# Optimization experiments

Measured on AMD Instinct MI355X. Metric: run time of the kernel, lower is better.

Reference implementation:

```python
import jax, jax.numpy as jnp
import numpy as np

PATCH, WIN = 3, 7


def _unfold(x, k):
    # torch F.unfold(x, k, padding=k//2), stride 1 -> [b, c, k*k, h, w]
    # channel-major ordering (c slowest, then kernel row, then kernel col)
    pad = k // 2
    b, c, h, w = x.shape
    xp = jnp.pad(x, ((0, 0), (0, 0), (pad, pad), (pad, pad)))
    return jnp.stack([xp[:, :, i:i + h, j:j + w]
                      for i in range(k) for j in range(k)], axis=2)


def _conv3(x, w, b=None):
    y = jax.lax.conv_general_dilated(x, w, (1, 1), [(1, 1), (1, 1)],
                                     dimension_numbers=('NCHW', 'OIHW', 'NCHW'))
    if b is not None:
        y = y + b[None, :, None, None]
    return y


def _head(u_feat, pan_feat, w_phi, w_theta, w_g, p, ws):
    # SelfAttention: windowed/patch neighborhood attention
    b, c, h, w = pan_feat.shape
    phi = jnp.einsum('oi,bihw->bohw', w_phi, pan_feat)
    theta = jnp.einsum('oi,bihw->bohw', w_theta, pan_feat)
    thp = _unfold(theta, p).reshape(b, c * p * p, h, w)        # [b,D,h,w]
    php = _unfold(phi, p).reshape(b, c * p * p, h, w)          # [b,D,h,w]
    phw = _unfold(php, ws)                                     # [b,D,K,h,w], K=ws*ws
    att = jax.nn.softmax(jnp.einsum('bdhw,bdkhw->bhwk', thp, phw), axis=-1)
    g = jnp.einsum('oi,bihw->bohw', w_g, u_feat)
    gw = _unfold(g, ws)                                        # [b,cu,K,h,w]
    return jnp.einsum('bhwk,bckhw->bchw', att, gw)


def _forward(u, pan, w_nlu, w_nlpan, g_phi, g_theta, g_g, s_phi, s_theta, s_g,
             m_phi, m_theta, m_g, mlp_w, mlp_b, w_resu, w_respan,
             rb0_w1, rb0_b1, rb0_w2, rb0_b2, rb1_w1, rb1_b1, rb1_w2, rb1_b2,
             rb2_w1, rb2_b1, rb2_w2, rb2_b2, w_recon):
    uf = _conv3(u, w_nlu)      # [b,5,h,w]
    pf = _conv3(pan, w_nlpan)  # [b,3,h,w]
    h1 = _head(uf, pf, g_phi, g_theta, g_g, PATCH, WIN)
    h2 = _head(uf, uf, s_phi, s_theta, s_g, 1, WIN)
    h3 = _head(uf, jnp.concatenate([uf, pf], axis=1), m_phi, m_theta, m_g, PATCH, WIN)
    # mlp: Linear(3,1) over stacked heads (last dim of size 3)
    att = h1 * mlp_w[0, 0] + h2 * mlp_w[0, 1] + h3 * mlp_w[0, 2] + mlp_b[0]
    ru = _conv3(u, w_resu)
    rp = _conv3(pan, w_respan)
    x = jnp.concatenate([att, ru, rp], axis=1)  # [b, fc+10, h, w]
    rbs = [(rb0_w1, rb0_b1, rb0_w2, rb0_b2),
           (rb1_w1, rb1_b1, rb1_w2, rb1_b2),
           (rb2_w1, rb2_b1, rb2_w2, rb2_b2)]
    for w1, b1, w2, b2 in rbs:
        f = jax.nn.relu(_conv3(x, w1, b1))
        f = _conv3(f, w2, b2)
        x = jax.nn.relu(f + x)
    return _conv3(x, w_recon)


def setup_inputs() -> dict:
    key = jax.random.key(0)
    ks = jax.random.split(key, 32)
    def n(i, shape, s=0.1):
        return jax.random.normal(ks[i], shape, dtype=jnp.float32) * s
    B, H, W = 1, 128, 128
    FC = 32
    C = FC + 10
    inp = {
        'u': jax.random.normal(ks[0], (B, 8, H, W), dtype=jnp.float32),
        'pan': jax.random.normal(ks[1], (B, 1, H, W), dtype=jnp.float32),
        'w_nlu': n(2, (5, 8, 3, 3)),
        'w_nlpan': n(3, (3, 1, 3, 3)),
        'g_phi': n(4, (3, 3)), 'g_theta': n(5, (3, 3)), 'g_g': n(6, (5, 5)),
        's_phi': n(7, (5, 5)), 's_theta': n(8, (5, 5)), 's_g': n(9, (5, 5)),
        'm_phi': n(10, (8, 8)), 'm_theta': n(11, (8, 8)), 'm_g': n(12, (5, 5)),
        'mlp_w': n(13, (1, 3), 0.5), 'mlp_b': n(14, (1,), 0.1),
        'w_resu': n(15, (FC, 8, 3, 3)), 'w_respan': n(16, (5, 1, 3, 3)),
        'w_recon': n(17, (8, C, 3, 3)),
    }
    k = 18
    for i in range(3):
        inp[f'rb{i}_w1'] = n(k, (C, C, 3, 3))
        inp[f'rb{i}_b1'] = n(k + 1, (C,), 0.01)
        inp[f'rb{i}_w2'] = n(k + 2, (C, C, 3, 3))
        inp[f'rb{i}_b2'] = n(k + 3, (C,), 0.01)
        k += 4
    return inp


def reference(u, pan, w_nlu, w_nlpan, g_phi, g_theta, g_g, s_phi, s_theta, s_g,
              m_phi, m_theta, m_g, mlp_w, mlp_b, w_resu, w_respan,
              rb0_w1, rb0_b1, rb0_w2, rb0_b2, rb1_w1, rb1_b1, rb1_w2, rb1_b2,
              rb2_w1, rb2_b1, rb2_w2, rb2_b2, w_recon):
    return _forward(u, pan, w_nlu, w_nlpan, g_phi, g_theta, g_g, s_phi, s_theta,
                    s_g, m_phi, m_theta, m_g, mlp_w, mlp_b, w_resu, w_respan,
                    rb0_w1, rb0_b1, rb0_w2, rb0_b2, rb1_w1, rb1_b1, rb1_w2,
                    rb1_b2, rb2_w1, rb2_b1, rb2_w2, rb2_b2, w_recon)
```

## Files before the change

### kernel.cpp

```cpp
#include <hip/hip_runtime.h>


#define DEV __device__ __forceinline__
typedef float f32x4 __attribute__((ext_vector_type(4)));
typedef __bf16 bf16x8 __attribute__((ext_vector_type(8)));
typedef unsigned short u16;
typedef unsigned int u32;

constexpr int N = 128 * 128;

constexpr int OFF_PHI1 =   0 * N;
constexpr int OFF_TH1  =   3 * N;
constexpr int OFF_PHI2 =   6 * N;
constexpr int OFF_TH2  =  11 * N;
constexpr int OFF_PHI3 =  16 * N;
constexpr int OFF_TH3  =  24 * N;
constexpr int OFF_G1   =  32 * N;
constexpr int OFF_G2   =  37 * N;
constexpr int OFF_G3   =  42 * N;
constexpr int OFF_X    =  47 * N;
constexpr int OFF_OH1  =  89 * N;
constexpr int OFF_OH2  =  94 * N;
constexpr int OFF_OH3  =  99 * N;
constexpr int XPLANE   = 130 * 136;
constexpr int OFF_XPAD = 110 * N;
constexpr int OFF_FPAD = 133 * N;
constexpr int OFF_SLAB = 156 * N;
constexpr int OFF_BTAB = 160 * N;
constexpr int SLAB_RB  = 18432;
constexpr int SLAB_RC  = 110592;
constexpr int SLAB_TOT = 116736;
constexpr int ZPB      = 528;
constexpr int ZTOT     = 2 * 42 * ZPB;
constexpr int WPREP_TOT = 384 + SLAB_TOT + ZTOT;
constexpr int WPREP_BLK = (WPREP_TOT + 255) / 256;

DEV bool inb(int y, int x) { return (unsigned)y < 128u && (unsigned)x < 128u; }
DEV u16 f2bf(float f) {
    unsigned u = __float_as_uint(f);
    return (u16)((u + 0x7fffu + ((u >> 16) & 1u)) >> 16);
}

struct PrepArgs {
    const float* u;    const float* pan;  const float* wnlu; const float* wnlpan;
    const float* gphi; const float* gth;  const float* gg;   const float* sphi;
    const float* sth;  const float* sg;   const float* mphi; const float* mth;
    const float* mg;
    const float* w[7];
};

__global__ __launch_bounds__(256) void prep_k(PrepArgs pa, float* __restrict__ ws,
                                              u16* __restrict__ slab,
                                              u16* __restrict__ btab,
                                              u16* __restrict__ xpad,
                                              u16* __restrict__ fpad) {
    const int bid = blockIdx.x, t = threadIdx.x;
    if (bid < 256) {
        const int g = bid >> 6;
        const int p = (bid & 63) * 256 + t;
        const int y = p >> 7, x = p & 127;

        float uv[8][9];
#pragma unroll
        for (int ic = 0; ic < 8; ++ic)
#pragma unroll
            for (int i = 0; i < 3; ++i)
#pragma unroll
                for (int j = 0; j < 3; ++j) {
                    int yy = y + i - 1, xx = x + j - 1;
                    uv[ic][i * 3 + j] =
                        inb(yy, xx) ? pa.u[ic * N + yy * 128 + xx] : 0.f;
                }
        float uf[5] = {0, 0, 0, 0, 0};
#pragma unroll
        for (int ic = 0; ic < 8; ++ic)
#pragma unroll
            for (int k = 0; k < 9; ++k)
#pragma unroll
                for (int o = 0; o < 5; ++o)
                    uf[o] = fmaf(uv[ic][k], pa.wnlu[(o * 8 + ic) * 9 + k], uf[o]);

        if (g == 0) {
#pragma unroll
            for (int o = 0; o < 5; ++o) {
                float a = 0, b = 0, c1 = 0;
#pragma unroll
                for (int i = 0; i < 5; ++i) {
                    a  = fmaf(pa.sphi[o * 5 + i], uf[i], a);
                    b  = fmaf(pa.sth [o * 5 + i], uf[i], b);
                    c1 = fmaf(pa.gg  [o * 5 + i], uf[i], c1);
                }
                ws[OFF_PHI2 + o * N + p] = a;
                ws[OFF_TH2  + o * N + p] = b;
                ws[OFF_G1   + o * N + p] = c1;
            }
        } else if (g == 1) {
#pragma unroll
            for (int o = 0; o < 5; ++o) {
                float c2 = 0, c3 = 0;
#pragma unroll
                for (int i = 0; i < 5; ++i) {
                    c2 = fmaf(pa.sg[o * 5 + i], uf[i], c2);
                    c3 = fmaf(pa.mg[o * 5 + i], uf[i], c3);
                }
                ws[OFF_G2 + o * N + p] = c2;
                ws[OFF_G3 + o * N + p] = c3;
            }
        } else {
            float pv[9];
#pragma unroll
            for (int i = 0; i < 3; ++i)
#pragma unroll
                for (int j = 0; j < 3; ++j) {
                    int yy = y + i - 1, xx = x + j - 1;
                    pv[i * 3 + j] = inb(yy, xx) ? pa.pan[yy * 128 + xx] : 0.f;
                }
            float pf[3] = {0, 0, 0};
#pragma unroll
            for (int k = 0; k < 9; ++k)
#pragma unroll
                for (int o = 0; o < 3; ++o)
                    pf[o] = fmaf(pv[k], pa.wnlpan[o * 9 + k], pf[o]);
            float cat[8] = {uf[0], uf[1], uf[2], uf[3], uf[4],
                            pf[0], pf[1], pf[2]};
            if (g == 2) {
#pragma unroll
                for (int o = 0; o < 3; ++o) {
                    float a = 0, b = 0;
#pragma unroll
                    for (int i = 0; i < 3; ++i) {
                        a = fmaf(pa.gphi[o * 3 + i], pf[i], a);
                        b = fmaf(pa.gth [o * 3 + i], pf[i], b);
                    }
                    ws[OFF_PHI1 + o * N + p] = a;
                    ws[OFF_TH1  + o * N + p] = b;
                }
#pragma unroll
                for (int o = 0; o < 8; ++o) {
                    float a = 0;
#pragma unroll
                    for (int i = 0; i < 8; ++i)
                        a = fmaf(pa.mphi[o * 8 + i], cat[i], a);
                    ws[OFF_PHI3 + o * N + p] = a;
                }
            } else {
#pragma unroll
                for (int o = 0; o < 8; ++o) {
                    float b = 0;
#pragma unroll
                    for (int i = 0; i < 8; ++i)
                        b = fmaf(pa.mth[o * 8 + i], cat[i], b);
                    ws[OFF_TH3 + o * N + p] = b;
                }
            }
        }
        return;
    }

    int idx = (bid - 256) * 256 + t;
    if (idx >= WPREP_TOT) return;
    if (idx < 384) {
        u16 v = 0;
        if (idx < 378) {
            int ic = idx / 9, tau = idx - ic * 9;
            v = (u16)(ic * 120 + (tau / 3) * 40 + (tau % 3));
        }
        btab[idx] = v;
        return;
    }
    idx -= 384;
    if (idx < SLAB_TOT) {
        const float* W;
        int mt, ks, lane, j, ocv;
        if (idx < SLAB_RC) {
            int cv = idx / SLAB_RB, r = idx - cv * SLAB_RB;
            mt = r / 6144; r -= mt * 6144;
            ks = r / 512;  r -= ks * 512;
            lane = r / 8;  j = r - lane * 8;
            W = pa.w[cv]; ocv = 42;
        } else {
            int r = idx - SLAB_RC;
            mt = 0;
            ks = r / 512;  r -= ks * 512;
            lane = r / 8;  j = r - lane * 8;
            W = pa.w[6]; ocv = 8;
        }
        int k  = ks * 32 + (lane >> 4) * 8 + j;
        int oc = mt * 16 + (lane & 15);
        u16 v = 0;
        if (k < 378 && oc < ocv) {
            int ic = k / 9, tau = k - ic * 9;
            v = f2bf(W[(oc * 42 + ic) * 9 + tau]);
        }
        slab[idx] = v;
        return;
    }
    idx -= SLAB_TOT;
    u16* buf = (idx < 42 * ZPB) ? xpad : fpad;
    int e = (idx < 42 * ZPB) ? idx : idx - 42 * ZPB;
    int plane = e / ZPB, rem = e - plane * ZPB;
    int row, col;
    if (rem < 136)      { row = 0;             col = rem; }
    else if (rem < 272) { row = 129;           col = rem - 136; }
    else if (rem < 400) { row = 1 + rem - 272; col = 0; }
    else                { row = 1 + rem - 400; col = 129; }
    buf[plane * XPLANE + row * 136 + col] = 0;
}

template <int C, int P>
DEV void head_tile(const float* __restrict__ phi, const float* __restrict__ theta,
                   const float* __restrict__ g, float* __restrict__ oh,
                   float* __restrict__ smem, int ty0, int tx0, int t) {
    constexpr int PR  = P / 2;
    constexpr int H3  = 3 + PR;
    constexpr int W   = 6 + P;
    constexpr int TTH = 8 + 2 * PR, TTW = 8 + 2 * PR;
    constexpr int PTH = 8 + 2 * H3, PTW = 8 + 2 * H3;
    constexpr int GTH = 14, GTW = 14;
    constexpr int CH0 = (C + 1) / 2;

    float* sT = smem;
    float* sP = sT + C * TTH * TTW;
    float* sG = sP + C * PTH * PTW;

#pragma unroll
    for (int c = 0; c < C; ++c) {
        int i = t;
        if (i < TTH * TTW) {
            int r = i / TTW, cc = i - r * TTW;
            int gy = ty0 - PR + r, gx = tx0 - PR + cc;
            sT[c * TTH * TTW + i] =
                inb(gy, gx) ? theta[c * N + gy * 128 + gx] : 0.f;
        }
    }
#pragma unroll
    for (int c = 0; c < C; ++c) {
        int i = t;
        if (i < PTH * PTW) {
            int r = i / PTW, cc = i - r * PTW;
            int gy = ty0 - H3 + r, gx = tx0 - H3 + cc;
            sP[c * PTH * PTW + i] =
                inb(gy, gx) ? phi[c * N + gy * 128 + gx] : 0.f;
        }
    }
#pragma unroll
    for (int c = 0; c < 5; ++c) {
        int i = t;
        if (i < GTH * GTW) {
            int r = i / GTW, cc = i - r * GTW;
            int gy = ty0 - 3 + r, gx = tx0 - 3 + cc;
            sG[c * GTH * GTW + i] =
                inb(gy, gx) ? g[c * N + gy * 128 + gx] : 0.f;
        }
    }
    __syncthreads();

    const int lane = t & 63, wave = t >> 6;
    const int h = (lane >> 4) & 1, m = lane >> 5;
    const int pidx = wave * 16 + (lane & 15);
    const int py = pidx >> 3, px = pidx & 7;
    const int gy = ty0 + py, gx = tx0 + px;
    const int dbase = m * 3;
    const int cbeg = h ? CH0 : 0, cend = h ? C : CH0;

    float s[28];
#pragma unroll
    for (int k = 0; k < 28; ++k) s[k] = 0.f;

#pragma unroll
    for (int ci = 0; ci < CH0; ++ci) {
        int c = cbeg + ci;
        bool cok = c < cend;
        const float* tc = sT + (cok ? c : 0) * TTH * TTW;
        const float* pc = sP + (cok ? c : 0) * PTH * PTW;
        float T[P][P];
#pragma unroll
        for (int i = 0; i < P; ++i)
#pragma unroll
            for (int j = 0; j < P; ++j)
                T[i][j] = cok ? tc[(py + i) * TTW + px + j] : 0.f;
        float R[P][W];
#pragma unroll
        for (int r = 0; r < P; ++r)
#pragma unroll
            for (int w = 0; w < W; ++w)
                R[r][w] = pc[(py + dbase + r) * PTW + px + w];
#pragma unroll
        for (int dd = 0; dd < 4; ++dd) {
#pragma unroll
            for (int dx = 0; dx < 7; ++dx) {
                float a = 0.f;
#pragma unroll
                for (int i = 0; i < P; ++i)
#pragma unroll
                    for (int j = 0; j < P; ++j)
                        a = fmaf(T[i][j], R[i][dx + j], a);
                s[dd * 7 + dx] += a;
            }
            if (dd < 3) {
#pragma unroll
                for (int r = 0; r < P - 1; ++r)
#pragma unroll
                    for (int w = 0; w < W; ++w) R[r][w] = R[r + 1][w];
                int row = py + dbase + dd + P;
#pragma unroll
                for (int w = 0; w < W; ++w)
                    R[P - 1][w] = pc[row * PTW + px + w];
            }
        }
    }
#pragma unroll
    for (int k = 0; k < 28; ++k) s[k] += __shfl_xor(s[k], 16);

#pragma unroll
    for (int k = 0; k < 28; ++k) {
        int d = dbase + k / 7, dx = k % 7;
        if (!inb(gy + d - 3, gx + dx - 3)) s[k] = 0.f;
    }
    const bool half0 = (m == 0);
    float mx = -3.0e38f;
#pragma unroll
    for (int k = 0; k < 28; ++k) {
        bool own = half0 || (k >= 7);
        mx = own ? fmaxf(mx, s[k]) : mx;
    }
    mx = fmaxf(mx, __shfl_xor(mx, 32));
    float sum = 0.f;
#pragma unroll
    for (int k = 0; k < 28; ++k) {
        bool own = half0 || (k >= 7);
        float e = own ? __expf(s[k] - mx) : 0.f;
        s[k] = e;
        sum += e;
    }
    sum += __shfl_xor(sum, 32);

    const int gb = h ? 3 : 0, gn = h ? 2 : 3;
    float o[3] = {0, 0, 0};
#pragma unroll
    for (int k = 0; k < 28; ++k) {
        int d = dbase + k / 7, dx = k % 7;
        int gr = (py + d) * GTW + px + dx;
#pragma unroll
        for (int c5 = 0; c5 < 3; ++c5)
            if (c5 < gn)
                o[c5] = fmaf(s[k], sG[(gb + c5) * GTH * GTW + gr], o[c5]);
    }
#pragma unroll
    for (int c5 = 0; c5 < 3; ++c5) o[c5] += __shfl_xor(o[c5], 32);

    if (half0) {
        float inv = 1.f / sum;
        int p = gy * 128 + gx;
#pragma unroll
        for (int c5 = 0; c5 < 3; ++c5)
            if (c5 < gn) oh[(gb + c5) * N + p] = o[c5] * inv;
    }
}

__global__ __launch_bounds__(256) void heads_k(float* __restrict__ ws) {
    __shared__ float smem[3828];
    const int t = threadIdx.x;
    const int ty0 = (blockIdx.x >> 4) * 8, tx0 = (blockIdx.x & 15) * 8;
    if (blockIdx.y == 0)
        head_tile<3, 3>(ws + OFF_PHI1, ws + OFF_TH1, ws + OFF_G1, ws + OFF_OH1,
                        smem, ty0, tx0, t);
    else if (blockIdx.y == 1)
        head_tile<5, 1>(ws + OFF_PHI2, ws + OFF_TH2, ws + OFF_G2, ws + OFF_OH2,
                        smem, ty0, tx0, t);
    else
        head_tile<8, 3>(ws + OFF_PHI3, ws + OFF_TH3, ws + OFF_G3, ws + OFF_OH3,
                        smem, ty0, tx0, t);
}

__global__ __launch_bounds__(256, 2) void assemble_k(
    const float* __restrict__ u, const float* __restrict__ pan,
    const float* __restrict__ wres, const float* __restrict__ wrp,
    const float* __restrict__ mlpw, const float* __restrict__ mlpb,
    float* __restrict__ ws, u16* __restrict__ xpad) {
    const int p = blockIdx.x * 256 + threadIdx.x;
    const int y = p >> 7, x = p & 127;
    const int padp = (y + 1) * 136 + (x + 1);
    float* xb = ws + OFF_X;

    if (blockIdx.y == 0) {
        const float w0 = mlpw[0], w1 = mlpw[1], w2 = mlpw[2];
        const float bb = mlpb[0];
#pragma unroll
        for (int c = 0; c < 5; ++c) {
            float a = ws[OFF_OH1 + c * N + p] * w0 +
                      ws[OFF_OH2 + c * N + p] * w1 +
                      ws[OFF_OH3 + c * N + p] * w2 + bb;
            xb[c * N + p] = a;
            xpad[c * XPLANE + padp] = f2bf(a);
        }
        float pv[9];
#pragma unroll
        for (int i = 0; i < 3; ++i)
#pragma unroll
            for (int j = 0; j < 3; ++j) {
                int yy = y + i - 1, xx = x + j - 1;
                pv[i * 3 + j] = inb(yy, xx) ? pan[yy * 128 + xx] : 0.f;
            }
        float a5[5] = {0, 0, 0, 0, 0};
#pragma unroll
        for (int k = 0; k < 9; ++k)
#pragma unroll
            for (int o = 0; o < 5; ++o)
                a5[o] = fmaf(pv[k], wrp[o * 9 + k], a5[o]);
#pragma unroll
        for (int o = 0; o < 5; ++o) {
            xb[(37 + o) * N + p] = a5[o];
            xpad[(37 + o) * XPLANE + padp] = f2bf(a5[o]);
        }
    } else {
        const int ob = (blockIdx.y - 1) * 8;
        float uv[8][9];
#pragma unroll
        for (int ic = 0; ic < 8; ++ic)
#pragma unroll
            for (int i = 0; i < 3; ++i)
#pragma unroll
                for (int j = 0; j < 3; ++j) {
                    int yy = y + i - 1, xx = x + j - 1;
                    uv[ic][i * 3 + j] =
                        inb(yy, xx) ? u[ic * N + yy * 128 + xx] : 0.f;
                }
        float acc[8] = {0, 0, 0, 0, 0, 0, 0, 0};
#pragma unroll
        for (int ic = 0; ic < 8; ++ic)
#pragma unroll
            for (int k = 0; k < 9; ++k)
#pragma unroll
                for (int o = 0; o < 8; ++o)
                    acc[o] = fmaf(uv[ic][k], wres[((ob + o) * 8 + ic) * 9 + k],
                                  acc[o]);
#pragma unroll
        for (int o = 0; o < 8; ++o) {
            xb[(5 + ob + o) * N + p] = acc[o];
            xpad[(5 + ob + o) * XPLANE + padp] = f2bf(acc[o]);
        }
    }
}

template <bool SKIP, bool WF32, bool WPAD>
__global__ __launch_bounds__(384, 3) void convm_k(
    const u16* __restrict__ xin, const u16* __restrict__ slab,
    const u16* __restrict__ btab, const float* __restrict__ bs,
    const float* __restrict__ skip, float* __restrict__ of32,
    u16* __restrict__ opad) {
    __shared__ __align__(16) u16 sX[5040];
    __shared__ __align__(16) u16 sBt[384];
    const int t = threadIdx.x;
    const int y = blockIdx.x >> 2, x0 = (blockIdx.x & 3) << 5;

    const u16* srcbase = xin + y * 136 + x0;
#pragma unroll
    for (int it = 0; it < 2; ++it) {
        int c = it * 384 + t;
        if (c < 630) {
            int row = c / 5, slot = c - row * 5;
            int ic = row / 3, r = row - ic * 3;
            uint4 v = *((const uint4*)(srcbase + ic * XPLANE + r * 136) + slot);
            *(uint4*)(sX + row * 40 + slot * 8) = v;
        }
    }
    sBt[t >= 384 ? 0 : t] = btab[t >= 384 ? 0 : t];
    __syncthreads();

    const int lane = t & 63, wave = t >> 6;
    const int ph = wave / 3, mt = wave - ph * 3;
    const int quad = lane >> 4, col = lane & 15;
    const int ncol = ph * 16 + col;

    union AB { uint4 u; bf16x8 b; };
    AB a[12];
#pragma unroll
    for (int ks = 0; ks < 12; ++ks)
        a[ks].u = ((const uint4*)slab)[(mt * 12 + ks) * 64 + lane];

    f32x4 acc = {0.f, 0.f, 0.f, 0.f};
#pragma unroll
    for (int ks = 0; ks < 12; ++ks) {
        union { uint4 u; u16 s[8]; } off;
        off.u = *(const uint4*)(sBt + ks * 32 + quad * 8);
        union { u16 s[8]; bf16x8 b; } bv;
#pragma unroll
        for (int j = 0; j < 8; ++j) bv.s[j] = sX[off.s[j] + ncol];
        acc = __builtin_amdgcn_mfma_f32_16x16x32_bf16(a[ks].b, bv.b, acc,
                                                      0, 0, 0);
    }

    const int xg = x0 + ncol;
    const int px = y * 128 + xg;
    const int padp = (y + 1) * 136 + (xg + 1);
#pragma unroll
    for (int reg = 0; reg < 4; ++reg) {
        int oc = mt * 16 + quad * 4 + reg;
        if (oc < 42) {
            float v = acc[reg] + bs[oc];
            if (SKIP) v += skip[oc * N + px];
            v = fmaxf(v, 0.f);
            if (WF32) of32[oc * N + px] = v;
            if (WPAD) opad[oc * XPLANE + padp] = f2bf(v);
        }
    }
}

__global__ __launch_bounds__(128, 1) void convr_k(
    const u16* __restrict__ xin, const u16* __restrict__ slab,
    const u16* __restrict__ btab, float* __restrict__ out) {
    __shared__ __align__(16) u16 sX[5040];
    __shared__ __align__(16) u16 sBt[384];
    const int t = threadIdx.x;
    const int y = blockIdx.x >> 2, x0 = (blockIdx.x & 3) << 5;

    const u16* srcbase = xin + y * 136 + x0;
#pragma unroll
    for (int it = 0; it < 5; ++it) {
        int c = it * 128 + t;
        if (c < 630) {
            int row = c / 5, slot = c - row * 5;
            int ic = row / 3, r = row - ic * 3;
            uint4 v = *((const uint4*)(srcbase + ic * XPLANE + r * 136) + slot);
            *(uint4*)(sX + row * 40 + slot * 8) = v;
        }
    }
#pragma unroll
    for (int it = 0; it < 3; ++it) sBt[it * 128 + t] = btab[it * 128 + t];
    __syncthreads();

    const int lane = t & 63, wave = t >> 6;
    const int quad = lane >> 4, col = lane & 15;
    const int ncol = wave * 16 + col;

    union AB { uint4 u; bf16x8 b; };
    AB a[12];
#pragma unroll
    for (int ks = 0; ks < 12; ++ks)
        a[ks].u = ((const uint4*)slab)[ks * 64 + lane];

    f32x4 acc = {0.f, 0.f, 0.f, 0.f};
#pragma unroll
    for (int ks = 0; ks < 12; ++ks) {
        union { uint4 u; u16 s[8]; } off;
        off.u = *(const uint4*)(sBt + ks * 32 + quad * 8);
        union { u16 s[8]; bf16x8 b; } bv;
#pragma unroll
        for (int j = 0; j < 8; ++j) bv.s[j] = sX[off.s[j] + ncol];
        acc = __builtin_amdgcn_mfma_f32_16x16x32_bf16(a[ks].b, bv.b, acc,
                                                      0, 0, 0);
    }
    const int px = y * 128 + x0 + ncol;
#pragma unroll
    for (int reg = 0; reg < 4; ++reg) {
        int oc = quad * 4 + reg;
        if (oc < 8) out[oc * N + px] = acc[reg];
    }
}

extern "C" void kernel_launch(void* const* d_in, const int* in_sizes, int n_in,
                              void* d_out, int out_size, void* d_ws, size_t ws_size,
                              hipStream_t stream) {
    (void)in_sizes; (void)n_in; (void)out_size; (void)ws_size;
    float* ws = (float*)d_ws;
    float* out = (float*)d_out;

    PrepArgs pa;
    pa.u      = (const float*)d_in[0];
    pa.pan    = (const float*)d_in[1];
    pa.wnlu   = (const float*)d_in[2];
    pa.wnlpan = (const float*)d_in[3];
    pa.gphi   = (const float*)d_in[4];
    pa.gth    = (const float*)d_in[5];
    pa.gg     = (const float*)d_in[6];
    pa.sphi   = (const float*)d_in[7];
    pa.sth    = (const float*)d_in[8];
    pa.sg     = (const float*)d_in[9];
    pa.mphi   = (const float*)d_in[10];
    pa.mth    = (const float*)d_in[11];
    pa.mg     = (const float*)d_in[12];
    pa.w[0]   = (const float*)d_in[18];
    pa.w[1]   = (const float*)d_in[20];
    pa.w[2]   = (const float*)d_in[22];
    pa.w[3]   = (const float*)d_in[24];
    pa.w[4]   = (const float*)d_in[26];
    pa.w[5]   = (const float*)d_in[28];
    pa.w[6]   = (const float*)d_in[17];

    const float* mlpw = (const float*)d_in[13];
    const float* mlpb = (const float*)d_in[14];
    const float* wres = (const float*)d_in[15];
    const float* wrp  = (const float*)d_in[16];

    u16* xpad = (u16*)(ws + OFF_XPAD);
    u16* fpad = (u16*)(ws + OFF_FPAD);
    u16* slab = (u16*)(ws + OFF_SLAB);
    u16* btab = (u16*)(ws + OFF_BTAB);

    prep_k<<<256 + WPREP_BLK, 256, 0, stream>>>(pa, ws, slab, btab, xpad, fpad);
    heads_k<<<dim3(256, 3), 256, 0, stream>>>(ws);
    assemble_k<<<dim3(64, 5), 256, 0, stream>>>(pa.u, pa.pan, wres, wrp, mlpw,
                                                mlpb, ws, xpad);

    for (int r = 0; r < 3; ++r) {
        const float* b1 = (const float*)d_in[19 + 4 * r];
        const float* b2 = (const float*)d_in[21 + 4 * r];
        convm_k<false, false, true>
            <<<512, 384, 0, stream>>>(xpad, slab + (2 * r) * SLAB_RB, btab, b1,
                                      nullptr, nullptr, fpad);
        convm_k<true, true, true>
            <<<512, 384, 0, stream>>>(fpad, slab + (2 * r + 1) * SLAB_RB, btab,
                                      b2, ws + OFF_X, ws + OFF_X, xpad);
    }
    convr_k<<<512, 128, 0, stream>>>(xpad, slab + SLAB_RC, btab, out);
}
```

Baseline: 208.9 us.

## Fuse residual block conv pairs into one kernel with halo recompute

Each residual block's two 3x3 convolutions now run in a single kernel. The first conv is computed over a 3x34 halo tile into shared memory, and the second conv reads it from there. The residual-branch convs move into the prep kernel, and the MLP head combine is folded into the first block, which removes the assemble kernel and the intermediate padded buffer round trip. The cost is redundant halo computation (102 vs 32 columns for the first conv), a wider 2-pixel padded layout, and more shared memory per block.

```diff
diff --git a/kernel.cpp b/kernel.cpp
--- a/kernel.cpp
+++ b/kernel.cpp
@@ -22,17 +22,17 @@
 constexpr int OFF_OH1  =  89 * N;
 constexpr int OFF_OH2  =  94 * N;
 constexpr int OFF_OH3  =  99 * N;
-constexpr int XPLANE   = 130 * 136;
-constexpr int OFF_XPAD = 110 * N;
-constexpr int OFF_FPAD = 133 * N;
-constexpr int OFF_SLAB = 156 * N;
-constexpr int OFF_BTAB = 160 * N;
+constexpr int XPLANE   = 132 * 144;
+constexpr int OFF_XPA  = 110 * N;
+constexpr int OFF_XPB  = 135 * N;
+constexpr int OFF_SLAB = 160 * N;
+constexpr int OFF_BTAB = 164 * N;
 constexpr int SLAB_RB  = 18432;
 constexpr int SLAB_RC  = 110592;
 constexpr int SLAB_TOT = 116736;
-constexpr int ZPB      = 528;
+constexpr int ZPB      = 2624;
 constexpr int ZTOT     = 2 * 42 * ZPB;
-constexpr int WPREP_TOT = 384 + SLAB_TOT + ZTOT;
+constexpr int WPREP_TOT = 1152 + SLAB_TOT + ZTOT;
 constexpr int WPREP_BLK = (WPREP_TOT + 255) / 256;
 
 DEV bool inb(int y, int x) { return (unsigned)y < 128u && (unsigned)x < 128u; }
@@ -45,15 +45,15 @@
     const float* u;    const float* pan;  const float* wnlu; const float* wnlpan;
     const float* gphi; const float* gth;  const float* gg;   const float* sphi;
     const float* sth;  const float* sg;   const float* mphi; const float* mth;
-    const float* mg;
+    const float* mg;   const float* wres; const float* wrp;
     const float* w[7];
 };
 
 __global__ __launch_bounds__(256) void prep_k(PrepArgs pa, float* __restrict__ ws,
                                               u16* __restrict__ slab,
                                               u16* __restrict__ btab,
-                                              u16* __restrict__ xpad,
-                                              u16* __restrict__ fpad) {
+                                              u16* __restrict__ xpa,
+                                              u16* __restrict__ xpb) {
     const int bid = blockIdx.x, t = threadIdx.x;
     if (bid < 256) {
         const int g = bid >> 6;
@@ -156,19 +156,79 @@
         }
         return;
     }
-
-    int idx = (bid - 256) * 256 + t;
+    if (bid < 576) {
+        const int ag = (bid - 256) >> 6;
+        const int p = ((bid - 256) & 63) * 256 + t;
+        const int y = p >> 7, x = p & 127;
+        const int padp = (y + 2) * 144 + (x + 2);
+        float* xb = ws + OFF_X;
+        if (ag == 0) {
+            float pv[9];
+#pragma unroll
+            for (int i = 0; i < 3; ++i)
+#pragma unroll
+                for (int j = 0; j < 3; ++j) {
+                    int yy = y + i - 1, xx = x + j - 1;
+                    pv[i * 3 + j] = inb(yy, xx) ? pa.pan[yy * 128 + xx] : 0.f;
+                }
+            float a5[5] = {0, 0, 0, 0, 0};
+#pragma unroll
+            for (int k = 0; k < 9; ++k)
+#pragma unroll
+                for (int o = 0; o < 5; ++o)
+                    a5[o] = fmaf(pv[k], pa.wrp[o * 9 + k], a5[o]);
+#pragma unroll
+            for (int o = 0; o < 5; ++o) {
+                xb[(37 + o) * N + p] = a5[o];
+                xpa[(37 + o) * XPLANE + padp] = f2bf(a5[o]);
+            }
+        } else {
+            const int ob = (ag - 1) * 8;
+            float uv[8][9];
+#pragma unroll
+            for (int ic = 0; ic < 8; ++ic)
+#pragma unroll
+                for (int i = 0; i < 3; ++i)
+#pragma unroll
+                    for (int j = 0; j < 3; ++j) {
+                        int yy = y + i - 1, xx = x + j - 1;
+                        uv[ic][i * 3 + j] =
+                            inb(yy, xx) ? pa.u[ic * N + yy * 128 + xx] : 0.f;
+                    }
+            float acc[8] = {0, 0, 0, 0, 0, 0, 0, 0};
+#pragma unroll
+            for (int ic = 0; ic < 8; ++ic)
+#pragma unroll
+                for (int k = 0; k < 9; ++k)
+#pragma unroll
+                    for (int o = 0; o < 8; ++o)
+                        acc[o] = fmaf(uv[ic][k],
+                                      pa.wres[((ob + o) * 8 + ic) * 9 + k],
+                                      acc[o]);
+#pragma unroll
+            for (int o = 0; o < 8; ++o) {
+                xb[(5 + ob + o) * N + p] = acc[o];
+                xpa[(5 + ob + o) * XPLANE + padp] = f2bf(acc[o]);
+            }
+        }
+        return;
+    }
+
+    int idx = (bid - 576) * 256 + t;
     if (idx >= WPREP_TOT) return;
-    if (idx < 384) {
+    if (idx < 1152) {
+        int which = idx / 384, k = idx - which * 384;
         u16 v = 0;
-        if (idx < 378) {
-            int ic = idx / 9, tau = idx - ic * 9;
-            v = (u16)(ic * 120 + (tau / 3) * 40 + (tau % 3));
+        if (k < 378) {
+            int ic = k / 9, tau = k - ic * 9, i = tau / 3, j = tau - i * 3;
+            if (which == 0)      v = (u16)(ic * 200 + i * 40 + j);
+            else if (which == 1) v = (u16)(ic * 120 + i * 40 + j);
+            else                 v = (u16)(ic * 120 + i * 40 + j + 1);
         }
         btab[idx] = v;
         return;
     }
-    idx -= 384;
+    idx -= 1152;
     if (idx < SLAB_TOT) {
         const float* W;
         int mt, ks, lane, j, ocv;
@@ -196,15 +256,21 @@
         return;
     }
     idx -= SLAB_TOT;
-    u16* buf = (idx < 42 * ZPB) ? xpad : fpad;
+    u16* buf = (idx < 42 * ZPB) ? xpa : xpb;
     int e = (idx < 42 * ZPB) ? idx : idx - 42 * ZPB;
     int plane = e / ZPB, rem = e - plane * ZPB;
     int row, col;
-    if (rem < 136)      { row = 0;             col = rem; }
-    else if (rem < 272) { row = 129;           col = rem - 136; }
-    else if (rem < 400) { row = 1 + rem - 272; col = 0; }
-    else                { row = 1 + rem - 400; col = 129; }
-    buf[plane * XPLANE + row * 136 + col] = 0;
+    if (rem < 576) {
+        int rr = rem / 144;
+        row = (rr < 2) ? rr : rr + 128;
+        col = rem - rr * 144;
+    } else {
+        int r2 = rem - 576;
+        row = 2 + r2 / 16;
+        int ci = r2 & 15;
+        col = (ci < 2) ? ci : 128 + ci;
+    }
+    buf[plane * XPLANE + row * 144 + col] = 0;
 }
 
 template <int C, int P>
@@ -373,136 +439,138 @@
                         smem, ty0, tx0, t);
 }
 
-__global__ __launch_bounds__(256, 2) void assemble_k(
-    const float* __restrict__ u, const float* __restrict__ pan,
-    const float* __restrict__ wres, const float* __restrict__ wrp,
-    const float* __restrict__ mlpw, const float* __restrict__ mlpb,
-    float* __restrict__ ws, u16* __restrict__ xpad) {
-    const int p = blockIdx.x * 256 + threadIdx.x;
-    const int y = p >> 7, x = p & 127;
-    const int padp = (y + 1) * 136 + (x + 1);
-    float* xb = ws + OFF_X;
-
-    if (blockIdx.y == 0) {
+template <bool COMBINE>
+__global__ __launch_bounds__(384, 2) void rbf_k(
+    const u16* __restrict__ xin, u16* __restrict__ xout,
+    const u16* __restrict__ slab1, const u16* __restrict__ slab2,
+    const u16* __restrict__ btab, const float* __restrict__ b1,
+    const float* __restrict__ b2, float* __restrict__ xskip,
+    const float* __restrict__ oh1, const float* __restrict__ oh2,
+    const float* __restrict__ oh3, const float* __restrict__ mlpw,
+    const float* __restrict__ mlpb) {
+    __shared__ __align__(16) u16 xT[8400];
+    __shared__ __align__(16) u16 fT[5040];
+    __shared__ __align__(16) u16 sBtA[384], sBtB[384];
+    __shared__ float sB1[42], sB2[42];
+    const int t = threadIdx.x;
+    const int y = blockIdx.x >> 2, x0 = (blockIdx.x & 3) << 5;
+
+    const u16* srcbase = xin + y * 144 + x0;
+    const int lo = COMBINE ? 5 : 0;
+    const int njobs = (42 - lo) * 5 * 5;
+#pragma unroll
+    for (int it = 0; it < 3; ++it) {
+        int c = it * 384 + t;
+        if (c < njobs) {
+            int row = c / 5, slot = c - row * 5;
+            int ic = lo + row / 5, r5 = row - (ic - lo) * 5;
+            uint4 v = *((const uint4*)(srcbase + ic * XPLANE + r5 * 144) + slot);
+            *(uint4*)(xT + ic * 200 + r5 * 40 + slot * 8) = v;
+        }
+    }
+    if (COMBINE) {
         const float w0 = mlpw[0], w1 = mlpw[1], w2 = mlpw[2];
         const float bb = mlpb[0];
-#pragma unroll
-        for (int c = 0; c < 5; ++c) {
-            float a = ws[OFF_OH1 + c * N + p] * w0 +
-                      ws[OFF_OH2 + c * N + p] * w1 +
-                      ws[OFF_OH3 + c * N + p] * w2 + bb;
-            xb[c * N + p] = a;
-            xpad[c * XPLANE + padp] = f2bf(a);
-        }
-        float pv[9];
-#pragma unroll
-        for (int i = 0; i < 3; ++i)
-#pragma unroll
-            for (int j = 0; j < 3; ++j) {
-                int yy = y + i - 1, xx = x + j - 1;
-                pv[i * 3 + j] = inb(yy, xx) ? pan[yy * 128 + xx] : 0.f;
-            }
-        float a5[5] = {0, 0, 0, 0, 0};
-#pragma unroll
-        for (int k = 0; k < 9; ++k)
-#pragma unroll
-            for (int o = 0; o < 5; ++o)
-                a5[o] = fmaf(pv[k], wrp[o * 9 + k], a5[o]);
-#pragma unroll
-        for (int o = 0; o < 5; ++o) {
-            xb[(37 + o) * N + p] = a5[o];
-            xpad[(37 + o) * XPLANE + padp] = f2bf(a5[o]);
-        }
-    } else {
-        const int ob = (blockIdx.y - 1) * 8;
-        float uv[8][9];
-#pragma unroll
-        for (int ic = 0; ic < 8; ++ic)
-#pragma unroll
-            for (int i = 0; i < 3; ++i)
-#pragma unroll
-                for (int j = 0; j < 3; ++j) {
-                    int yy = y + i - 1, xx = x + j - 1;
-                    uv[ic][i * 3 + j] =
-                        inb(yy, xx) ? u[ic * N + yy * 128 + xx] : 0.f;
-                }
-        float acc[8] = {0, 0, 0, 0, 0, 0, 0, 0};
-#pragma unroll
-        for (int ic = 0; ic < 8; ++ic)
-#pragma unroll
-            for (int k = 0; k < 9; ++k)
-#pragma unroll
-                for (int o = 0; o < 8; ++o)
-                    acc[o] = fmaf(uv[ic][k], wres[((ob + o) * 8 + ic) * 9 + k],
-                                  acc[o]);
-#pragma unroll
-        for (int o = 0; o < 8; ++o) {
-            xb[(5 + ob + o) * N + p] = acc[o];
-            xpad[(5 + ob + o) * XPLANE + padp] = f2bf(acc[o]);
-        }
-    }
-}
-
-template <bool SKIP, bool WF32, bool WPAD>
-__global__ __launch_bounds__(384, 3) void convm_k(
-    const u16* __restrict__ xin, const u16* __restrict__ slab,
-    const u16* __restrict__ btab, const float* __restrict__ bs,
-    const float* __restrict__ skip, float* __restrict__ of32,
-    u16* __restrict__ opad) {
-    __shared__ __align__(16) u16 sX[5040];
-    __shared__ __align__(16) u16 sBt[384];
-    const int t = threadIdx.x;
-    const int y = blockIdx.x >> 2, x0 = (blockIdx.x & 3) << 5;
-
-    const u16* srcbase = xin + y * 136 + x0;
-#pragma unroll
-    for (int it = 0; it < 2; ++it) {
-        int c = it * 384 + t;
-        if (c < 630) {
-            int row = c / 5, slot = c - row * 5;
-            int ic = row / 3, r = row - ic * 3;
-            uint4 v = *((const uint4*)(srcbase + ic * XPLANE + r * 136) + slot);
-            *(uint4*)(sX + row * 40 + slot * 8) = v;
-        }
-    }
-    sBt[t >= 384 ? 0 : t] = btab[t >= 384 ? 0 : t];
+        if (t < 200) {
+            int rr = t / 40, cc = t - rr * 40;
+            int iy = y - 2 + rr, ix = x0 - 2 + cc;
+            if (inb(iy, ix)) {
+                int p = iy * 128 + ix;
+#pragma unroll
+                for (int c5 = 0; c5 < 5; ++c5) {
+                    float a = oh1[c5 * N + p] * w0 + oh2[c5 * N + p] * w1 +
+                              oh3[c5 * N + p] * w2 + bb;
+                    xT[c5 * 200 + rr * 40 + cc] = f2bf(a);
+                }
+            } else {
+#pragma unroll
+                for (int c5 = 0; c5 < 5; ++c5)
+                    xT[c5 * 200 + rr * 40 + cc] = 0;
+            }
+        }
+    }
+    sBtA[t] = btab[t];
+    sBtB[t] = btab[384 + t];
+    if (t < 42) { sB1[t] = b1[t]; sB2[t] = b2[t]; }
     __syncthreads();
 
     const int lane = t & 63, wave = t >> 6;
-    const int ph = wave / 3, mt = wave - ph * 3;
     const int quad = lane >> 4, col = lane & 15;
-    const int ncol = ph * 16 + col;
 
     union AB { uint4 u; bf16x8 b; };
-    AB a[12];
-#pragma unroll
-    for (int ks = 0; ks < 12; ++ks)
-        a[ks].u = ((const uint4*)slab)[(mt * 12 + ks) * 64 + lane];
-
-    f32x4 acc = {0.f, 0.f, 0.f, 0.f};
-#pragma unroll
-    for (int ks = 0; ks < 12; ++ks) {
-        union { uint4 u; u16 s[8]; } off;
-        off.u = *(const uint4*)(sBt + ks * 32 + quad * 8);
-        union { u16 s[8]; bf16x8 b; } bv;
-#pragma unroll
-        for (int j = 0; j < 8; ++j) bv.s[j] = sX[off.s[j] + ncol];
-        acc = __builtin_amdgcn_mfma_f32_16x16x32_bf16(a[ks].b, bv.b, acc,
-                                                      0, 0, 0);
-    }
-
-    const int xg = x0 + ncol;
-    const int px = y * 128 + xg;
-    const int padp = (y + 1) * 136 + (xg + 1);
-#pragma unroll
-    for (int reg = 0; reg < 4; ++reg) {
-        int oc = mt * 16 + quad * 4 + reg;
-        if (oc < 42) {
-            float v = acc[reg] + bs[oc];
-            if (SKIP) v += skip[oc * N + px];
-            v = fmaxf(v, 0.f);
-            if (WF32) of32[oc * N + px] = v;
-            if (WPAD) opad[oc * XPLANE + padp] = f2bf(v);
+
+    for (int job = wave; job < 21; job += 6) {
+        int tile = job / 3, mt = job - 3 * tile;
+        int n = tile * 16 + col;
+        bool vn = n < 102;
+        int r = vn ? n / 34 : 0, c = vn ? n - (n / 34) * 34 : 0;
+        int base = r * 40 + c;
+        AB a[12];
+#pragma unroll
+        for (int ks = 0; ks < 12; ++ks)
+            a[ks].u = ((const uint4*)slab1)[(mt * 12 + ks) * 64 + lane];
+        f32x4 acc = {0.f, 0.f, 0.f, 0.f};
+#pragma unroll
+        for (int ks = 0; ks < 12; ++ks) {
+            union { uint4 u; u16 s[8]; } off;
+            off.u = *(const uint4*)(sBtA + ks * 32 + quad * 8);
+            union { u16 s[8]; bf16x8 b; } bv;
+#pragma unroll
+            for (int j = 0; j < 8; ++j) bv.s[j] = xT[off.s[j] + base];
+            acc = __builtin_amdgcn_mfma_f32_16x16x32_bf16(a[ks].b, bv.b, acc,
+                                                          0, 0, 0);
+        }
+        int gy = y - 1 + r, gxx = x0 - 1 + c;
+        bool img = inb(gy, gxx);
+#pragma unroll
+        for (int reg = 0; reg < 4; ++reg) {
+            int oc = mt * 16 + quad * 4 + reg;
+            if (oc < 42 && vn) {
+                float v = fmaxf(acc[reg] + sB1[oc], 0.f);
+                fT[oc * 120 + r * 40 + c] = img ? f2bf(v) : (u16)0;
+            }
+        }
+    }
+    __syncthreads();
+
+    {
+        int ph = wave / 3, mt = wave - 3 * ph;
+        int ncol = ph * 16 + col;
+        AB a[12];
+#pragma unroll
+        for (int ks = 0; ks < 12; ++ks)
+            a[ks].u = ((const uint4*)slab2)[(mt * 12 + ks) * 64 + lane];
+        f32x4 acc = {0.f, 0.f, 0.f, 0.f};
+#pragma unroll
+        for (int ks = 0; ks < 12; ++ks) {
+            union { uint4 u; u16 s[8]; } off;
+            off.u = *(const uint4*)(sBtB + ks * 32 + quad * 8);
+            union { u16 s[8]; bf16x8 b; } bv;
+#pragma unroll
+            for (int j = 0; j < 8; ++j) bv.s[j] = fT[off.s[j] + ncol];
+            acc = __builtin_amdgcn_mfma_f32_16x16x32_bf16(a[ks].b, bv.b, acc,
+                                                          0, 0, 0);
+        }
+        int xg = x0 + ncol;
+        int px = y * 128 + xg;
+        int padp = (y + 2) * 144 + (xg + 2);
+#pragma unroll
+        for (int reg = 0; reg < 4; ++reg) {
+            int oc = mt * 16 + quad * 4 + reg;
+            if (oc < 42) {
+                float v = acc[reg] + sB2[oc];
+                float sk;
+                if (COMBINE && oc < 5) {
+                    sk = oh1[oc * N + px] * mlpw[0] + oh2[oc * N + px] * mlpw[1] +
+                         oh3[oc * N + px] * mlpw[2] + mlpb[0];
+                } else {
+                    sk = xskip[oc * N + px];
+                }
+                v += sk;
+                v = fmaxf(v, 0.f);
+                xskip[oc * N + px] = v;
+                xout[oc * XPLANE + padp] = f2bf(v);
+            }
         }
     }
 }
@@ -515,19 +583,19 @@
     const int t = threadIdx.x;
     const int y = blockIdx.x >> 2, x0 = (blockIdx.x & 3) << 5;
 
-    const u16* srcbase = xin + y * 136 + x0;
+    const u16* srcbase = xin + (y + 1) * 144 + x0;
 #pragma unroll
     for (int it = 0; it < 5; ++it) {
         int c = it * 128 + t;
         if (c < 630) {
             int row = c / 5, slot = c - row * 5;
             int ic = row / 3, r = row - ic * 3;
-            uint4 v = *((const uint4*)(srcbase + ic * XPLANE + r * 136) + slot);
+            uint4 v = *((const uint4*)(srcbase + ic * XPLANE + r * 144) + slot);
             *(uint4*)(sX + row * 40 + slot * 8) = v;
         }
     }
 #pragma unroll
-    for (int it = 0; it < 3; ++it) sBt[it * 128 + t] = btab[it * 128 + t];
+    for (int it = 0; it < 3; ++it) sBt[it * 128 + t] = btab[768 + it * 128 + t];
     __syncthreads();
 
     const int lane = t & 63, wave = t >> 6;
@@ -580,6 +648,8 @@
     pa.mphi   = (const float*)d_in[10];
     pa.mth    = (const float*)d_in[11];
     pa.mg     = (const float*)d_in[12];
+    pa.wres   = (const float*)d_in[15];
+    pa.wrp    = (const float*)d_in[16];
     pa.w[0]   = (const float*)d_in[18];
     pa.w[1]   = (const float*)d_in[20];
     pa.w[2]   = (const float*)d_in[22];
@@ -590,28 +660,29 @@
 
     const float* mlpw = (const float*)d_in[13];
     const float* mlpb = (const float*)d_in[14];
-    const float* wres = (const float*)d_in[15];
-    const float* wrp  = (const float*)d_in[16];
-
-    u16* xpad = (u16*)(ws + OFF_XPAD);
-    u16* fpad = (u16*)(ws + OFF_FPAD);
+
+    u16* xpa  = (u16*)(ws + OFF_XPA);
+    u16* xpb  = (u16*)(ws + OFF_XPB);
     u16* slab = (u16*)(ws + OFF_SLAB);
     u16* btab = (u16*)(ws + OFF_BTAB);
-
-    prep_k<<<256 + WPREP_BLK, 256, 0, stream>>>(pa, ws, slab, btab, xpad, fpad);
+    float* oh1 = ws + OFF_OH1;
+    float* oh2 = ws + OFF_OH2;
+    float* oh3 = ws + OFF_OH3;
+
+    prep_k<<<576 + WPREP_BLK, 256, 0, stream>>>(pa, ws, slab, btab, xpa, xpb);
     heads_k<<<dim3(256, 3), 256, 0, stream>>>(ws);
-    assemble_k<<<dim3(64, 5), 256, 0, stream>>>(pa.u, pa.pan, wres, wrp, mlpw,
-                                                mlpb, ws, xpad);
-
-    for (int r = 0; r < 3; ++r) {
-        const float* b1 = (const float*)d_in[19 + 4 * r];
-        const float* b2 = (const float*)d_in[21 + 4 * r];
-        convm_k<false, false, true>
-            <<<512, 384, 0, stream>>>(xpad, slab + (2 * r) * SLAB_RB, btab, b1,
-                                      nullptr, nullptr, fpad);
-        convm_k<true, true, true>
-            <<<512, 384, 0, stream>>>(fpad, slab + (2 * r + 1) * SLAB_RB, btab,
-                                      b2, ws + OFF_X, ws + OFF_X, xpad);
-    }
-    convr_k<<<512, 128, 0, stream>>>(xpad, slab + SLAB_RC, btab, out);
+
+    rbf_k<true><<<512, 384, 0, stream>>>(
+        xpa, xpb, slab + 0 * SLAB_RB, slab + 1 * SLAB_RB, btab,
+        (const float*)d_in[19], (const float*)d_in[21], ws + OFF_X,
+        oh1, oh2, oh3, mlpw, mlpb);
+    rbf_k<false><<<512, 384, 0, stream>>>(
+        xpb, xpa, slab + 2 * SLAB_RB, slab + 3 * SLAB_RB, btab,
+        (const float*)d_in[23], (const float*)d_in[25], ws + OFF_X,
+        oh1, oh2, oh3, mlpw, mlpb);
+    rbf_k<false><<<512, 384, 0, stream>>>(
+        xpa, xpb, slab + 4 * SLAB_RB, slab + 5 * SLAB_RB, btab,
+        (const float*)d_in[27], (const float*)d_in[29], ws + OFF_X,
+        oh1, oh2, oh3, mlpw, mlpb);
+    convr_k<<<512, 128, 0, stream>>>(xpb, slab + SLAB_RC, btab, out);
 }
```

Result: slower. 214.0 us (+2.4%).
